# Optimization experiments

Measured on AMD Instinct MI355X. Metric: run time of the kernel, lower is better.

Reference implementation:

```python
import jax, jax.numpy as jnp
import numpy as np

B, N, L, K, C1 = 128, 300, 600, 19, 100  # batch, num_cnns, input_length, filter_size, fc hidden
PS = 7  # pool size == stride
LC = L - (K - 1)               # 582, conv output length
LP = (LC - PS) // PS + 1       # 83, pooled length
NC = 2                         # num_classes
EPS = 1e-5


def _bn(x, g, b, m, v):
    # eval-mode batchnorm, params broadcast along given axes already
    return g * (x - m) * jax.lax.rsqrt(v + EPS) + b


def setup_inputs() -> dict:
    key = jax.random.key(0)
    ks = jax.random.split(key, 20)
    f = lambda i, shape, s=0.1: (jax.random.normal(ks[i], shape, dtype=jnp.float32) * s)
    pv = lambda i, shape: (jax.random.uniform(ks[i], shape, dtype=jnp.float32) + 0.5)
    return {
        'x': jax.random.normal(ks[0], (B, 4, L), dtype=jnp.float32),
        'conv_w': f(1, (N, 4, K)), 'conv_b': f(2, (N,)),
        'bn1_g': pv(3, (N,)), 'bn1_b': f(4, (N,)), 'bn1_m': f(5, (N,)), 'bn1_v': pv(6, (N,)),
        'fc1_w': f(7, (N, C1, LP)), 'fc1_b': f(8, (N, C1)),
        'bn2_g': pv(9, (N, C1)), 'bn2_b': f(10, (N, C1)), 'bn2_m': f(11, (N, C1)), 'bn2_v': pv(12, (N, C1)),
        'fc2_w': f(13, (N, C1)), 'fc2_b': f(14, (N,)),
        'bn3_g': pv(15, (N,)), 'bn3_b': f(16, (N,)), 'bn3_m': f(17, (N,)), 'bn3_v': pv(18, (N,)),
        'final_w': f(19, (NC, N)), 'final_b': jnp.zeros((NC,), dtype=jnp.float32),
    }


def reference(x, conv_w, conv_b, bn1_g, bn1_b, bn1_m, bn1_v,
              fc1_w, fc1_b, bn2_g, bn2_b, bn2_m, bn2_v,
              fc2_w, fc2_b, bn3_g, bn3_b, bn3_m, bn3_v,
              final_w, final_b):
    # grouped conv on a repeated input == plain conv with 4 in-channels, N out-channels
    h = jax.lax.conv_general_dilated(x, conv_w, window_strides=(1,), padding='VALID',
                                     dimension_numbers=('NCH', 'OIH', 'NCH'))  # [B,N,582]
    h = h + conv_b[None, :, None]
    h = _bn(h, bn1_g[None, :, None], bn1_b[None, :, None], bn1_m[None, :, None], bn1_v[None, :, None])
    h = jnp.exp(h)
    # MaxPool1d(7,7): [B,N,582] -> [B,N,83]
    h = jax.lax.reduce_window(h, -jnp.inf, jax.lax.max,
                              window_dimensions=(1, 1, PS), window_strides=(1, 1, PS), padding='VALID')
    # grouped 1x1 conv == per-unit dense: [B,N,83] x [N,100,83] -> [B,N,100]
    h = jnp.einsum('bnp,nhp->bnh', h, fc1_w) + fc1_b[None]
    h = jax.nn.relu(_bn(h, bn2_g[None], bn2_b[None], bn2_m[None], bn2_v[None]))
    # second grouped 1x1 conv: [B,N,100] x [N,100] -> [B,N]
    h = jnp.einsum('bnh,nh->bn', h, fc2_w) + fc2_b[None]
    h = jax.nn.relu(_bn(h, bn3_g[None], bn3_b[None], bn3_m[None], bn3_v[None]))
    return h @ final_w.T + final_b  # [B,num_classes]
```

## Files before the change

kernel.cpp:

```cpp
#include <hip/hip_runtime.h>
#include <math.h>

#define EPS_ 1e-5f

__global__ __launch_bounds__(256) void kP(const float* __restrict__ fc1w,
                                          const float* __restrict__ conv_w,
                                          float* __restrict__ w1T,
                                          float* __restrict__ cwT) {
    __shared__ float sm[22800];
    const int blk = blockIdx.x, tid = threadIdx.x;
    if (blk < 300) {
        for (int i = tid; i < 8300; i += 256) {
            const int h = i / 83, p = i - h * 83;
            sm[p * 101 + h] = fc1w[(size_t)blk * 8300 + i];
        }
        __syncthreads();
        for (int i = tid; i < 8300; i += 256) {
            const int p = i / 100, h = i - p * 100;
            w1T[(size_t)blk * 8300 + i] = sm[p * 101 + h];
        }
    } else {
        for (int i = tid; i < 22800; i += 256) sm[i] = conv_w[i];
        __syncthreads();
        for (int i = tid; i < 22800; i += 256) {
            const int k = i / 300, n = i - k * 300;
            cwT[i] = sm[n * 76 + k];
        }
    }
}

__global__ __launch_bounds__(64) void kA(
        const float* __restrict__ x,
        const float* __restrict__ cwT,
        const float* __restrict__ conv_b,
        const float* __restrict__ g1, const float* __restrict__ b1,
        const float* __restrict__ m1, const float* __restrict__ v1,
        float* __restrict__ pooled)
{
    const int id  = blockIdx.x;
    const int b   = id / 40;
    const int sub = id - b * 40;
    const int ng  = sub >> 3;
    const int pc  = sub & 7;
    const int p0  = (pc * 83) >> 3;
    const int p1  = ((pc + 1) * 83) >> 3;
    const int lane = threadIdx.x;
    const int n   = ng * 64 + lane;
    const int nc  = (n < 300) ? n : 299;

    float w[4][19];
    #pragma unroll
    for (int c = 0; c < 4; ++c)
        #pragma unroll
        for (int k = 0; k < 19; ++k)
            w[c][k] = cwT[(c * 19 + k) * 300 + nc];

    const float A1 = g1[nc] * rsqrtf(v1[nc] + EPS_);
    const float B1 = fmaf(A1, conv_b[nc] - m1[nc], b1[nc]);

    const float* xb = x + b * 2400;

    for (int p = p0; p < p1; ++p) {
        const int t0 = 7 * p;
        float acc[7];
        #pragma unroll
        for (int q = 0; q < 7; ++q) acc[q] = 0.f;

        #pragma unroll
        for (int c = 0; c < 4; ++c) {
            const float* xc = xb + c * 600 + t0;
            float xv[25];
            #pragma unroll
            for (int j = 0; j < 25; ++j) xv[j] = xc[j];
            #pragma unroll
            for (int k = 0; k < 19; ++k) {
                const float wv = w[c][k];
                #pragma unroll
                for (int q = 0; q < 7; ++q)
                    acc[q] = fmaf(xv[k + q], wv, acc[q]);
            }
        }
        float mx = -INFINITY;
        #pragma unroll
        for (int q = 0; q < 7; ++q) mx = fmaxf(mx, fmaf(A1, acc[q], B1));
        if (n < 300)
            pooled[((size_t)n * 83 + p) * 128 + b] = __expf(mx);
    }
}

__global__ __launch_bounds__(128) void kB(
        const float* __restrict__ pooled,
        const float* __restrict__ w1T,
        const float* __restrict__ fc1b,
        const float* __restrict__ g2, const float* __restrict__ b2,
        const float* __restrict__ m2, const float* __restrict__ v2,
        const float* __restrict__ fc2w,
        const float* __restrict__ fc2b,
        const float* __restrict__ g3, const float* __restrict__ b3,
        const float* __restrict__ m3, const float* __restrict__ v3,
        float* __restrict__ sout)
{
    __shared__ float sRed[2][16];
    const int id = blockIdx.x;
    const int bc = id / 304;
    const int n  = id - bc * 304;
    if (n >= 300) return;
    const int tid  = threadIdx.x;
    const int lane = tid & 63;
    const int hw   = tid >> 6;
    const int lc   = (lane < 50) ? lane : 49;
    const int h    = hw * 50 + lc;
    const int b0   = bc * 16;

    const float* wp = w1T + (size_t)n * 8300 + h;
    const float* pp = pooled + (size_t)n * 83 * 128 + b0;

    float acc[16];
    #pragma unroll
    for (int i = 0; i < 16; ++i) acc[i] = 0.f;

    #pragma unroll 4
    for (int p = 0; p < 83; ++p) {
        const float wv = wp[p * 100];
        const float4 s0 = *reinterpret_cast<const float4*>(pp + p * 128 + 0);
        const float4 s1 = *reinterpret_cast<const float4*>(pp + p * 128 + 4);
        const float4 s2 = *reinterpret_cast<const float4*>(pp + p * 128 + 8);
        const float4 s3 = *reinterpret_cast<const float4*>(pp + p * 128 + 12);
        acc[ 0] = fmaf(s0.x, wv, acc[ 0]);  acc[ 1] = fmaf(s0.y, wv, acc[ 1]);
        acc[ 2] = fmaf(s0.z, wv, acc[ 2]);  acc[ 3] = fmaf(s0.w, wv, acc[ 3]);
        acc[ 4] = fmaf(s1.x, wv, acc[ 4]);  acc[ 5] = fmaf(s1.y, wv, acc[ 5]);
        acc[ 6] = fmaf(s1.z, wv, acc[ 6]);  acc[ 7] = fmaf(s1.w, wv, acc[ 7]);
        acc[ 8] = fmaf(s2.x, wv, acc[ 8]);  acc[ 9] = fmaf(s2.y, wv, acc[ 9]);
        acc[10] = fmaf(s2.z, wv, acc[10]);  acc[11] = fmaf(s2.w, wv, acc[11]);
        acc[12] = fmaf(s3.x, wv, acc[12]);  acc[13] = fmaf(s3.y, wv, acc[13]);
        acc[14] = fmaf(s3.z, wv, acc[14]);  acc[15] = fmaf(s3.w, wv, acc[15]);
    }

    const int hi = n * 100 + h;
    const float A2  = g2[hi] * rsqrtf(v2[hi] + EPS_);
    const float C2  = fmaf(A2, fc1b[hi] - m2[hi], b2[hi]);
    const float w2m = (lane < 50) ? fc2w[hi] : 0.f;

    float part[16];
    #pragma unroll
    for (int i = 0; i < 16; ++i)
        part[i] = fmaxf(fmaf(A2, acc[i], C2), 0.f) * w2m;

    #pragma unroll
    for (int off = 32; off > 0; off >>= 1)
        #pragma unroll
        for (int i = 0; i < 16; ++i)
            part[i] += __shfl_xor(part[i], off, 64);

    if (lane == 0) {
        #pragma unroll
        for (int i = 0; i < 16; ++i) sRed[hw][i] = part[i];
    }
    __syncthreads();
    if (tid < 16) {
        float s = sRed[0][tid] + sRed[1][tid] + fc2b[n];
        const float A3 = g3[n] * rsqrtf(v3[n] + EPS_);
        const float z = fmaf(A3, s - m3[n], b3[n]);
        sout[n * 128 + b0 + tid] = fmaxf(z, 0.f);
    }
}

__global__ __launch_bounds__(64) void kC(
        const float* __restrict__ sout,
        const float* __restrict__ fw,
        const float* __restrict__ fb,
        float* __restrict__ out)
{
    const int b = blockIdx.x, t = threadIdx.x;
    float a0 = 0.f, a1 = 0.f;
    for (int nn = t; nn < 300; nn += 64) {
        const float v = sout[nn * 128 + b];
        a0 = fmaf(v, fw[nn], a0);
        a1 = fmaf(v, fw[300 + nn], a1);
    }
    #pragma unroll
    for (int off = 32; off > 0; off >>= 1) {
        a0 += __shfl_xor(a0, off, 64);
        a1 += __shfl_xor(a1, off, 64);
    }
    if (t == 0) {
        out[b * 2 + 0] = a0 + fb[0];
        out[b * 2 + 1] = a1 + fb[1];
    }
}

extern "C" void kernel_launch(void* const* d_in, const int* in_sizes, int n_in,
                              void* d_out, int out_size, void* d_ws, size_t ws_size,
                              hipStream_t stream) {
    const float* x      = (const float*)d_in[0];
    const float* conv_w = (const float*)d_in[1];
    const float* conv_b = (const float*)d_in[2];
    const float* g1 = (const float*)d_in[3];
    const float* b1 = (const float*)d_in[4];
    const float* m1 = (const float*)d_in[5];
    const float* v1 = (const float*)d_in[6];
    const float* fc1_w = (const float*)d_in[7];
    const float* fc1_b = (const float*)d_in[8];
    const float* g2 = (const float*)d_in[9];
    const float* b2 = (const float*)d_in[10];
    const float* m2 = (const float*)d_in[11];
    const float* v2 = (const float*)d_in[12];
    const float* fc2_w = (const float*)d_in[13];
    const float* fc2_b = (const float*)d_in[14];
    const float* g3 = (const float*)d_in[15];
    const float* b3 = (const float*)d_in[16];
    const float* m3 = (const float*)d_in[17];
    const float* v3 = (const float*)d_in[18];
    const float* fw = (const float*)d_in[19];
    const float* fb = (const float*)d_in[20];
    float* out = (float*)d_out;

    float* pooled = (float*)d_ws;
    float* w1T    = pooled + (size_t)300 * 83 * 128;
    float* cwT    = w1T + (size_t)300 * 8300;
    float* sout   = cwT + 22800;

    kP<<<301, 256, 0, stream>>>(fc1_w, conv_w, w1T, cwT);
    kA<<<5120, 64, 0, stream>>>(x, cwT, conv_b, g1, b1, m1, v1, pooled);
    kB<<<2432, 128, 0, stream>>>(pooled, w1T, fc1_b, g2, b2, m2, v2,
                                 fc2_w, fc2_b, g3, b3, m3, v3, sout);
    kC<<<128, 64, 0, stream>>>(sout, fw, fb, out);
}
```

Measured before the change: 198.9 us.

## Register-block conv over four pooled outputs and remap FC1 lanes to batch

In the conv kernel each thread now computes four consecutive pooled outputs from one shared 46-element input window per channel. The last chunk is clamped so it overlaps its neighbour. The aim is to reuse input loads and cut loop overhead, at the cost of more accumulator registers. The FC1 kernel now maps lanes to batch elements, and each thread keeps 50 hidden accumulators fed by wave-uniform weight loads. This removes the cross-lane shuffle reduction but launches far fewer blocks and uses more registers per thread.

Result: faster. 189.8 us (-4.6%).

```diff
diff --git a/kernel.cpp b/kernel.cpp
--- a/kernel.cpp
+++ b/kernel.cpp
@@ -38,53 +38,51 @@
         float* __restrict__ pooled)
 {
     const int id  = blockIdx.x;
-    const int b   = id / 40;
-    const int sub = id - b * 40;
-    const int ng  = sub >> 3;
-    const int pc  = sub & 7;
-    const int p0  = (pc * 83) >> 3;
-    const int p1  = ((pc + 1) * 83) >> 3;
+    const int b   = id / 112;
+    const int sub = id - b * 112;
+    if (sub >= 105) return;
+    const int ng  = sub / 21;
+    const int pc  = sub - ng * 21;
+    const int p0c = pc * 4;
+    const int p0  = (p0c > 79) ? 79 : p0c;
     const int lane = threadIdx.x;
     const int n   = ng * 64 + lane;
     const int nc  = (n < 300) ? n : 299;
 
-    float w[4][19];
-    #pragma unroll
-    for (int c = 0; c < 4; ++c)
-        #pragma unroll
-        for (int k = 0; k < 19; ++k)
-            w[c][k] = cwT[(c * 19 + k) * 300 + nc];
+    float acc[28];
+    #pragma unroll
+    for (int i = 0; i < 28; ++i) acc[i] = 0.f;
+
+    #pragma unroll 1
+    for (int c = 0; c < 4; ++c) {
+        const float* xc = x + b * 2400 + c * 600 + 7 * p0;
+        float xw[46];
+        #pragma unroll
+        for (int j = 0; j < 46; ++j) xw[j] = xc[j];
+        const float* wc = cwT + c * 19 * 300 + nc;
+        #pragma unroll
+        for (int k = 0; k < 19; ++k) {
+            const float wv = wc[k * 300];
+            #pragma unroll
+            for (int p = 0; p < 4; ++p)
+                #pragma unroll
+                for (int q = 0; q < 7; ++q)
+                    acc[p * 7 + q] = fmaf(xw[7 * p + q + k], wv, acc[p * 7 + q]);
+        }
+    }
 
     const float A1 = g1[nc] * rsqrtf(v1[nc] + EPS_);
     const float B1 = fmaf(A1, conv_b[nc] - m1[nc], b1[nc]);
-
-    const float* xb = x + b * 2400;
-
-    for (int p = p0; p < p1; ++p) {
-        const int t0 = 7 * p;
-        float acc[7];
-        #pragma unroll
-        for (int q = 0; q < 7; ++q) acc[q] = 0.f;
-
-        #pragma unroll
-        for (int c = 0; c < 4; ++c) {
-            const float* xc = xb + c * 600 + t0;
-            float xv[25];
+    if (n < 300) {
+        float* op = pooled + ((size_t)n * 83 + p0) * 128 + b;
+        #pragma unroll
+        for (int p = 0; p < 4; ++p) {
+            float mx = -INFINITY;
             #pragma unroll
-            for (int j = 0; j < 25; ++j) xv[j] = xc[j];
-            #pragma unroll
-            for (int k = 0; k < 19; ++k) {
-                const float wv = w[c][k];
-                #pragma unroll
-                for (int q = 0; q < 7; ++q)
-                    acc[q] = fmaf(xv[k + q], wv, acc[q]);
-            }
-        }
-        float mx = -INFINITY;
-        #pragma unroll
-        for (int q = 0; q < 7; ++q) mx = fmaxf(mx, fmaf(A1, acc[q], B1));
-        if (n < 300)
-            pooled[((size_t)n * 83 + p) * 128 + b] = __expf(mx);
+            for (int q = 0; q < 7; ++q)
+                mx = fmaxf(mx, fmaf(A1, acc[p * 7 + q], B1));
+            op[p * 128] = __expf(mx);
+        }
     }
 }
 
@@ -100,68 +98,48 @@
         const float* __restrict__ m3, const float* __restrict__ v3,
         float* __restrict__ sout)
 {
-    __shared__ float sRed[2][16];
+    __shared__ float sRed[2][64];
     const int id = blockIdx.x;
-    const int bc = id / 304;
-    const int n  = id - bc * 304;
+    const int bh = id / 304;
+    const int n  = id - bh * 304;
     if (n >= 300) return;
     const int tid  = threadIdx.x;
     const int lane = tid & 63;
-    const int hw   = tid >> 6;
-    const int lc   = (lane < 50) ? lane : 49;
-    const int h    = hw * 50 + lc;
-    const int b0   = bc * 16;
-
-    const float* wp = w1T + (size_t)n * 8300 + h;
-    const float* pp = pooled + (size_t)n * 83 * 128 + b0;
-
-    float acc[16];
-    #pragma unroll
-    for (int i = 0; i < 16; ++i) acc[i] = 0.f;
-
-    #pragma unroll 4
+    const int hh   = __builtin_amdgcn_readfirstlane(tid >> 6);
+    const int h0   = hh * 50;
+    const int bb   = bh * 64 + lane;
+
+    const float* pp = pooled + (size_t)n * 83 * 128 + bb;
+    const float* wp = w1T + (size_t)n * 8300 + h0;
+
+    float acc[50];
+    #pragma unroll
+    for (int j = 0; j < 50; ++j) acc[j] = 0.f;
+
+    #pragma unroll 2
     for (int p = 0; p < 83; ++p) {
-        const float wv = wp[p * 100];
-        const float4 s0 = *reinterpret_cast<const float4*>(pp + p * 128 + 0);
-        const float4 s1 = *reinterpret_cast<const float4*>(pp + p * 128 + 4);
-        const float4 s2 = *reinterpret_cast<const float4*>(pp + p * 128 + 8);
-        const float4 s3 = *reinterpret_cast<const float4*>(pp + p * 128 + 12);
-        acc[ 0] = fmaf(s0.x, wv, acc[ 0]);  acc[ 1] = fmaf(s0.y, wv, acc[ 1]);
-        acc[ 2] = fmaf(s0.z, wv, acc[ 2]);  acc[ 3] = fmaf(s0.w, wv, acc[ 3]);
-        acc[ 4] = fmaf(s1.x, wv, acc[ 4]);  acc[ 5] = fmaf(s1.y, wv, acc[ 5]);
-        acc[ 6] = fmaf(s1.z, wv, acc[ 6]);  acc[ 7] = fmaf(s1.w, wv, acc[ 7]);
-        acc[ 8] = fmaf(s2.x, wv, acc[ 8]);  acc[ 9] = fmaf(s2.y, wv, acc[ 9]);
-        acc[10] = fmaf(s2.z, wv, acc[10]);  acc[11] = fmaf(s2.w, wv, acc[11]);
-        acc[12] = fmaf(s3.x, wv, acc[12]);  acc[13] = fmaf(s3.y, wv, acc[13]);
-        acc[14] = fmaf(s3.z, wv, acc[14]);  acc[15] = fmaf(s3.w, wv, acc[15]);
-    }
-
-    const int hi = n * 100 + h;
-    const float A2  = g2[hi] * rsqrtf(v2[hi] + EPS_);
-    const float C2  = fmaf(A2, fc1b[hi] - m2[hi], b2[hi]);
-    const float w2m = (lane < 50) ? fc2w[hi] : 0.f;
-
-    float part[16];
-    #pragma unroll
-    for (int i = 0; i < 16; ++i)
-        part[i] = fmaxf(fmaf(A2, acc[i], C2), 0.f) * w2m;
-
-    #pragma unroll
-    for (int off = 32; off > 0; off >>= 1)
-        #pragma unroll
-        for (int i = 0; i < 16; ++i)
-            part[i] += __shfl_xor(part[i], off, 64);
-
-    if (lane == 0) {
-        #pragma unroll
-        for (int i = 0; i < 16; ++i) sRed[hw][i] = part[i];
-    }
+        const float pv = pp[p * 128];
+        #pragma unroll
+        for (int j = 0; j < 50; ++j)
+            acc[j] = fmaf(pv, wp[p * 100 + j], acc[j]);
+    }
+
+    const int base = n * 100 + h0;
+    float part = 0.f;
+    #pragma unroll
+    for (int j = 0; j < 50; ++j) {
+        const float A2 = g2[base + j] * rsqrtf(v2[base + j] + EPS_);
+        const float C2 = fmaf(A2, fc1b[base + j] - m2[base + j], b2[base + j]);
+        const float act = fmaxf(fmaf(A2, acc[j], C2), 0.f);
+        part = fmaf(act, fc2w[base + j], part);
+    }
+    sRed[hh][lane] = part;
     __syncthreads();
-    if (tid < 16) {
+    if (tid < 64) {
         float s = sRed[0][tid] + sRed[1][tid] + fc2b[n];
         const float A3 = g3[n] * rsqrtf(v3[n] + EPS_);
         const float z = fmaf(A3, s - m3[n], b3[n]);
-        sout[n * 128 + b0 + tid] = fmaxf(z, 0.f);
+        sout[n * 128 + bh * 64 + tid] = fmaxf(z, 0.f);
     }
 }
 
@@ -221,8 +199,8 @@
     float* sout   = cwT + 22800;
 
     kP<<<301, 256, 0, stream>>>(fc1_w, conv_w, w1T, cwT);
-    kA<<<5120, 64, 0, stream>>>(x, cwT, conv_b, g1, b1, m1, v1, pooled);
-    kB<<<2432, 128, 0, stream>>>(pooled, w1T, fc1_b, g2, b2, m2, v2,
-                                 fc2_w, fc2_b, g3, b3, m3, v3, sout);
+    kA<<<128 * 112, 64, 0, stream>>>(x, cwT, conv_b, g1, b1, m1, v1, pooled);
+    kB<<<608, 128, 0, stream>>>(pooled, w1T, fc1_b, g2, b2, m2, v2,
+                                fc2_w, fc2_b, g3, b3, m3, v3, sout);
     kC<<<128, 64, 0, stream>>>(sout, fw, fb, out);
 }
```
